# Optimization experiments

Measured on AMD Instinct MI355X. Metric: run time of the kernel, lower is better.

Reference implementation:

```python
import jax, jax.numpy as jnp
import numpy as np

NUM_NEGATIVES = 5  # global in original script
# TUPLE_OPTION == 'average', DATATYPE != 'clique' (tuplewise branch active)


def setup_inputs() -> dict:
    key = jax.random.key(0)
    k1, k2, k3 = jax.random.split(key, 3)
    N, D, P = 50000, 128, 8
    Q = NUM_NEGATIVES * P  # assert pos*NUM_NEGATIVES == neg in original
    return {
        "node_features": jax.random.normal(k1, (N, D), dtype=jnp.float32),
        "pos_idx": jax.random.randint(k2, (N, P), 0, N),
        "neg_idx": jax.random.randint(k3, (N, Q), 0, N),
        "hyperedge_node_idx": 10000,
    }


def reference(node_features, pos_idx, neg_idx, hyperedge_node_idx):
    x = node_features                      # [N, D]
    N = x.shape[0]
    P = pos_idx.shape[1]
    Q = neg_idx.shape[1]
    # per-node dot products with gathered neighbors, then sigmoid
    pos_s = jax.nn.sigmoid(jnp.einsum('nd,npd->np', x, x[pos_idx]))  # [N, P]
    neg_s = jax.nn.sigmoid(jnp.einsum('nd,nqd->nq', x, x[neg_idx]))  # [N, Q]
    # NOTE: original applies BCE-with-logits ON TOP of sigmoid scores (double
    # sigmoid) -- kept faithful. bce_logits(s, y) = softplus(s) - s*y
    per_node_pair = (
        (jax.nn.softplus(pos_s) - pos_s).sum(axis=1)  # labels = 1
        + jax.nn.softplus(neg_s).sum(axis=1)          # labels = 0
    ) / (P + Q)
    pairwise_loss = per_node_pair.mean()

    # tuplewise: reshape negs to (NUM_NEGATIVES, P) per node, average (TUPLE_OPTION='average')
    pos_t = pos_s.mean(axis=1)                                   # [N]
    neg_t = neg_s.reshape(N, NUM_NEGATIVES, P).mean(axis=2)      # [N, NUM_NEGATIVES]
    per_node_tuple = (
        jax.nn.softplus(pos_t) - pos_t
        + jax.nn.softplus(neg_t).sum(axis=1)
    ) / (1 + NUM_NEGATIVES)
    tuplewise_loss = per_node_tuple.sum() / (N - hyperedge_node_idx)

    return pairwise_loss + tuplewise_loss
```

## Files before the change

### kernel.cpp

```cpp
#include <hip/hip_runtime.h>

#define DIMS   128
#define PNUM   8
#define QNUM   40
#define NBR    48
#define WAVES_PER_BLOCK 4

typedef float f2 __attribute__((ext_vector_type(2)));

__global__ __launch_bounds__(256) void convert_f32_to_f8(
    const float* __restrict__ x, unsigned int* __restrict__ x8, int n8)
{
    const int stride = gridDim.x * blockDim.x;
    for (int i = blockIdx.x * blockDim.x + threadIdx.x; i < n8; i += stride) {
        const float4 v0 = reinterpret_cast<const float4*>(x)[2 * i];
        const float4 v1 = reinterpret_cast<const float4*>(x)[2 * i + 1];
        unsigned int a = __builtin_amdgcn_cvt_pk_fp8_f32(v0.x, v0.y, 0u, false);
        a = __builtin_amdgcn_cvt_pk_fp8_f32(v0.z, v0.w, a, true);
        unsigned int b = __builtin_amdgcn_cvt_pk_fp8_f32(v1.x, v1.y, 0u, false);
        b = __builtin_amdgcn_cvt_pk_fp8_f32(v1.z, v1.w, b, true);
        uint2 o; o.x = a; o.y = b;
        reinterpret_cast<uint2*>(x8)[i] = o;
    }
}

__device__ __forceinline__ float node_epilogue(float s, int lane, int N, int h)
{
    float pair_part = 0.0f;
    if (lane < NBR) {
        const float sp = __logf(1.0f + __expf(s));
        pair_part = (lane < PNUM) ? (sp - s) : sp;
    }
    float gs = s;
    gs += __shfl_xor(gs, 1);
    gs += __shfl_xor(gs, 2);
    gs += __shfl_xor(gs, 4);

    float tuple_part = 0.0f;
    if ((lane & 7) == 0 && lane < NBR) {
        const float t  = gs * 0.125f;
        const float sp = __logf(1.0f + __expf(t));
        tuple_part = (lane == 0) ? (sp - t) : sp;
    }
    const float pair_scale  = 1.0f / (48.0f * (float)N);
    const float tuple_scale = 1.0f / (6.0f  * (float)(N - h));
    return pair_part * pair_scale + tuple_part * tuple_scale;
}

__global__ __launch_bounds__(256) void node_loss_partial_f8v3(
    const float*        __restrict__ x,
    const unsigned int* __restrict__ x8,
    const int*          __restrict__ pos_idx,
    const int*          __restrict__ neg_idx,
    const int*          __restrict__ h_ptr,
    float*              __restrict__ ws,
    int N)
{
    __shared__ float scores_sh[WAVES_PER_BLOCK][NBR];
    __shared__ float wsum[WAVES_PER_BLOCK];

    const int wave = threadIdx.x >> 6;
    const int lane = threadIdx.x & 63;
    const int sub  = lane & 7;
    const int grp  = lane >> 3;
    const int node = blockIdx.x * WAVES_PER_BLOCK + wave;

    const int h = *h_ptr;

    float v = 0.0f;
    if (node < N) {
        int nb[6];
        nb[0] = pos_idx[node * PNUM + grp];
#pragma unroll
        for (int p = 1; p < 6; ++p)
            nb[p] = neg_idx[node * QNUM + (p - 1) * 8 + grp];

        const float4* own =
            reinterpret_cast<const float4*>(x + (size_t)node * DIMS) + sub * 4;
        const float4 f0 = own[0], f1 = own[1], f2v = own[2], f3 = own[3];

        uint4 q[6];
#pragma unroll
        for (int p = 0; p < 6; ++p)
            q[p] = *reinterpret_cast<const uint4*>(x8 + (size_t)nb[p] * 32 + sub * 4);

        f2 A2[8];
        A2[0] = f2{f0.x, f0.y};   A2[1] = f2{f0.z, f0.w};
        A2[2] = f2{f1.x, f1.y};   A2[3] = f2{f1.z, f1.w};
        A2[4] = f2{f2v.x, f2v.y}; A2[5] = f2{f2v.z, f2v.w};
        A2[6] = f2{f3.x, f3.y};   A2[7] = f2{f3.z, f3.w};

#pragma unroll
        for (int p = 0; p < 6; ++p) {
            f2 acc2 = {0.0f, 0.0f};
            acc2 += __builtin_amdgcn_cvt_pk_f32_fp8(q[p].x, false) * A2[0];
            acc2 += __builtin_amdgcn_cvt_pk_f32_fp8(q[p].x, true)  * A2[1];
            acc2 += __builtin_amdgcn_cvt_pk_f32_fp8(q[p].y, false) * A2[2];
            acc2 += __builtin_amdgcn_cvt_pk_f32_fp8(q[p].y, true)  * A2[3];
            acc2 += __builtin_amdgcn_cvt_pk_f32_fp8(q[p].z, false) * A2[4];
            acc2 += __builtin_amdgcn_cvt_pk_f32_fp8(q[p].z, true)  * A2[5];
            acc2 += __builtin_amdgcn_cvt_pk_f32_fp8(q[p].w, false) * A2[6];
            acc2 += __builtin_amdgcn_cvt_pk_f32_fp8(q[p].w, true)  * A2[7];
            float acc = acc2[0] + acc2[1];
            acc += __shfl_xor(acc, 1);
            acc += __shfl_xor(acc, 2);
            acc += __shfl_xor(acc, 4);
            if (sub == 0) scores_sh[wave][p * 8 + grp] = acc;
        }

        float s = 0.0f;
        if (lane < NBR) {
            const float sc = scores_sh[wave][lane];
            s = __builtin_amdgcn_rcpf(1.0f + __expf(-sc));
        }
        v = node_epilogue(s, lane, N, h);
    }

    v += __shfl_xor(v, 1);
    v += __shfl_xor(v, 2);
    v += __shfl_xor(v, 4);
    v += __shfl_xor(v, 8);
    v += __shfl_xor(v, 16);
    v += __shfl_xor(v, 32);

    if (lane == 0) wsum[wave] = v;
    __syncthreads();
    if (threadIdx.x == 0)
        ws[blockIdx.x] = wsum[0] + wsum[1] + wsum[2] + wsum[3];
}

__global__ __launch_bounds__(256) void node_loss_partial_f32(
    const float* __restrict__ x,
    const int*   __restrict__ pos_idx,
    const int*   __restrict__ neg_idx,
    const int*   __restrict__ h_ptr,
    float*       __restrict__ ws,
    int N)
{
    __shared__ float xn_sh[WAVES_PER_BLOCK][DIMS];
    __shared__ float wsum[WAVES_PER_BLOCK];

    const int wave = threadIdx.x >> 6;
    const int lane = threadIdx.x & 63;
    const int node = blockIdx.x * WAVES_PER_BLOCK + wave;

    if (node < N && lane < 32) {
        const float4* row = reinterpret_cast<const float4*>(x + (size_t)node * DIMS);
        reinterpret_cast<float4*>(xn_sh[wave])[lane] = row[lane];
    }
    __syncthreads();

    float v = 0.0f;
    if (node < N) {
        float s = 0.0f;
        if (lane < NBR) {
            const int nb = (lane < PNUM)
                ? pos_idx[node * PNUM + lane]
                : neg_idx[node * QNUM + (lane - PNUM)];
            const float4* nrow = reinterpret_cast<const float4*>(x + (size_t)nb * DIMS);
            const float4* xn4  = reinterpret_cast<const float4*>(xn_sh[wave]);
            float acc = 0.0f;
#pragma unroll
            for (int t = 0; t < DIMS / 4; ++t) {
                const float4 a = xn4[t];
                const float4 b = nrow[t];
                acc += a.x * b.x + a.y * b.y + a.z * b.z + a.w * b.w;
            }
            s = 1.0f / (1.0f + expf(-acc));
        }
        v = node_epilogue(s, lane, N, *h_ptr);
    }

    v += __shfl_xor(v, 1);
    v += __shfl_xor(v, 2);
    v += __shfl_xor(v, 4);
    v += __shfl_xor(v, 8);
    v += __shfl_xor(v, 16);
    v += __shfl_xor(v, 32);

    if (lane == 0) wsum[wave] = v;
    __syncthreads();
    if (threadIdx.x == 0)
        ws[blockIdx.x] = wsum[0] + wsum[1] + wsum[2] + wsum[3];
}

__global__ __launch_bounds__(256) void reduce_final(
    const float* __restrict__ ws, float* __restrict__ out, int nparts)
{
    __shared__ float sm[WAVES_PER_BLOCK];
    float acc = 0.0f;
    for (int i = threadIdx.x; i < nparts; i += 256) acc += ws[i];

    acc += __shfl_xor(acc, 1);
    acc += __shfl_xor(acc, 2);
    acc += __shfl_xor(acc, 4);
    acc += __shfl_xor(acc, 8);
    acc += __shfl_xor(acc, 16);
    acc += __shfl_xor(acc, 32);

    const int wave = threadIdx.x >> 6;
    const int lane = threadIdx.x & 63;
    if (lane == 0) sm[wave] = acc;
    __syncthreads();
    if (threadIdx.x == 0)
        out[0] = sm[0] + sm[1] + sm[2] + sm[3];
}

extern "C" void kernel_launch(void* const* d_in, const int* in_sizes, int n_in,
                              void* d_out, int out_size, void* d_ws, size_t ws_size,
                              hipStream_t stream) {
    const float* x   = (const float*)d_in[0];
    const int*   pos = (const int*)d_in[1];
    const int*   neg = (const int*)d_in[2];
    const int*   h   = (const int*)d_in[3];

    const int N = in_sizes[0] / DIMS;
    const int nblocks = (N + WAVES_PER_BLOCK - 1) / WAVES_PER_BLOCK;

    const size_t x8_bytes = (size_t)N * DIMS;
    const size_t need     = x8_bytes + (size_t)nblocks * sizeof(float);

    if (ws_size >= need) {
        unsigned int* x8 = (unsigned int*)d_ws;
        float* partials  = (float*)((char*)d_ws + x8_bytes);
        const int n8 = N * DIMS / 8;
        convert_f32_to_f8<<<2048, 256, 0, stream>>>(x, x8, n8);
        node_loss_partial_f8v3<<<nblocks, 256, 0, stream>>>(x, x8, pos, neg, h, partials, N);
        reduce_final<<<1, 256, 0, stream>>>(partials, (float*)d_out, nblocks);
    } else {
        float* partials = (float*)d_ws;
        node_loss_partial_f32<<<nblocks, 256, 0, stream>>>(x, pos, neg, h, partials, N);
        reduce_final<<<1, 256, 0, stream>>>(partials, (float*)d_out, nblocks);
    }
}
```

Baseline: 54.42 us.

## Compute per-node neighbor dot products with FP8 MFMA instead of VALU unpacking

Replaces the per-lane FP8 unpack-and-FMA dot products with 16x16x32 FP8 MFMA instructions. Each wave computes 48 neighbor scores as three 16-column tiles, reading the diagonal accumulator element, so the shared-memory score staging and shuffle reductions go away. The node's own row is now read from the FP8 copy rather than FP32, which cuts gather traffic but adds quantization error on both operands. The MFMA tiles compute a 16x16 product where only one row is needed, so most of the matrix work is discarded.

```diff
diff --git a/kernel.cpp b/kernel.cpp
--- a/kernel.cpp
+++ b/kernel.cpp
@@ -6,7 +6,7 @@
 #define NBR    48
 #define WAVES_PER_BLOCK 4
 
-typedef float f2 __attribute__((ext_vector_type(2)));
+typedef float f32x4 __attribute__((ext_vector_type(4)));
 
 __global__ __launch_bounds__(256) void convert_f32_to_f8(
     const float* __restrict__ x, unsigned int* __restrict__ x8, int n8)
@@ -47,70 +47,76 @@
     return pair_part * pair_scale + tuple_part * tuple_scale;
 }
 
-__global__ __launch_bounds__(256) void node_loss_partial_f8v3(
-    const float*        __restrict__ x,
-    const unsigned int* __restrict__ x8,
-    const int*          __restrict__ pos_idx,
-    const int*          __restrict__ neg_idx,
-    const int*          __restrict__ h_ptr,
-    float*              __restrict__ ws,
+__global__ __launch_bounds__(256) void node_loss_mfma_wave(
+    const unsigned char* __restrict__ x8,
+    const int*           __restrict__ pos_idx,
+    const int*           __restrict__ neg_idx,
+    const int*           __restrict__ h_ptr,
+    float*               __restrict__ ws,
     int N)
 {
-    __shared__ float scores_sh[WAVES_PER_BLOCK][NBR];
     __shared__ float wsum[WAVES_PER_BLOCK];
 
     const int wave = threadIdx.x >> 6;
     const int lane = threadIdx.x & 63;
-    const int sub  = lane & 7;
-    const int grp  = lane >> 3;
+    const int col  = lane & 15;
+    const int q    = lane >> 4;
     const int node = blockIdx.x * WAVES_PER_BLOCK + wave;
 
     const int h = *h_ptr;
 
     float v = 0.0f;
     if (node < N) {
-        int nb[6];
-        nb[0] = pos_idx[node * PNUM + grp];
-#pragma unroll
-        for (int p = 1; p < 6; ++p)
-            nb[p] = neg_idx[node * QNUM + (p - 1) * 8 + grp];
-
-        const float4* own =
-            reinterpret_cast<const float4*>(x + (size_t)node * DIMS) + sub * 4;
-        const float4 f0 = own[0], f1 = own[1], f2v = own[2], f3 = own[3];
-
-        uint4 q[6];
-#pragma unroll
-        for (int p = 0; p < 6; ++p)
-            q[p] = *reinterpret_cast<const uint4*>(x8 + (size_t)nb[p] * 32 + sub * 4);
-
-        f2 A2[8];
-        A2[0] = f2{f0.x, f0.y};   A2[1] = f2{f0.z, f0.w};
-        A2[2] = f2{f1.x, f1.y};   A2[3] = f2{f1.z, f1.w};
-        A2[4] = f2{f2v.x, f2v.y}; A2[5] = f2{f2v.z, f2v.w};
-        A2[6] = f2{f3.x, f3.y};   A2[7] = f2{f3.z, f3.w};
-
-#pragma unroll
-        for (int p = 0; p < 6; ++p) {
-            f2 acc2 = {0.0f, 0.0f};
-            acc2 += __builtin_amdgcn_cvt_pk_f32_fp8(q[p].x, false) * A2[0];
-            acc2 += __builtin_amdgcn_cvt_pk_f32_fp8(q[p].x, true)  * A2[1];
-            acc2 += __builtin_amdgcn_cvt_pk_f32_fp8(q[p].y, false) * A2[2];
-            acc2 += __builtin_amdgcn_cvt_pk_f32_fp8(q[p].y, true)  * A2[3];
-            acc2 += __builtin_amdgcn_cvt_pk_f32_fp8(q[p].z, false) * A2[4];
-            acc2 += __builtin_amdgcn_cvt_pk_f32_fp8(q[p].z, true)  * A2[5];
-            acc2 += __builtin_amdgcn_cvt_pk_f32_fp8(q[p].w, false) * A2[6];
-            acc2 += __builtin_amdgcn_cvt_pk_f32_fp8(q[p].w, true)  * A2[7];
-            float acc = acc2[0] + acc2[1];
-            acc += __shfl_xor(acc, 1);
-            acc += __shfl_xor(acc, 2);
-            acc += __shfl_xor(acc, 4);
-            if (sub == 0) scores_sh[wave][p * 8 + grp] = acc;
-        }
+        const int nb0 = (col < PNUM) ? pos_idx[node * PNUM + col]
+                                     : neg_idx[node * QNUM + (col - PNUM)];
+        const int nb1 = neg_idx[node * QNUM + 8 + col];
+        const int nb2 = neg_idx[node * QNUM + 24 + col];
+
+        const unsigned char* ap = x8 + (size_t)node * DIMS + q * 32;
+        const ulonglong2 a01 = *reinterpret_cast<const ulonglong2*>(ap);
+        const ulonglong2 a23 = *reinterpret_cast<const ulonglong2*>(ap + 16);
+
+        const unsigned char* b0p = x8 + (size_t)nb0 * DIMS + q * 32;
+        const unsigned char* b1p = x8 + (size_t)nb1 * DIMS + q * 32;
+        const unsigned char* b2p = x8 + (size_t)nb2 * DIMS + q * 32;
+        const ulonglong2 b0a = *reinterpret_cast<const ulonglong2*>(b0p);
+        const ulonglong2 b0b = *reinterpret_cast<const ulonglong2*>(b0p + 16);
+        const ulonglong2 b1a = *reinterpret_cast<const ulonglong2*>(b1p);
+        const ulonglong2 b1b = *reinterpret_cast<const ulonglong2*>(b1p + 16);
+        const ulonglong2 b2a = *reinterpret_cast<const ulonglong2*>(b2p);
+        const ulonglong2 b2b = *reinterpret_cast<const ulonglong2*>(b2p + 16);
+
+        f32x4 acc0 = {0.f, 0.f, 0.f, 0.f};
+        f32x4 acc1 = {0.f, 0.f, 0.f, 0.f};
+        f32x4 acc2 = {0.f, 0.f, 0.f, 0.f};
+        acc0 = __builtin_amdgcn_mfma_f32_16x16x32_fp8_fp8(
+            (long long)a01.x, (long long)b0a.x, acc0, 0, 0, 0);
+        acc1 = __builtin_amdgcn_mfma_f32_16x16x32_fp8_fp8(
+            (long long)a01.x, (long long)b1a.x, acc1, 0, 0, 0);
+        acc2 = __builtin_amdgcn_mfma_f32_16x16x32_fp8_fp8(
+            (long long)a01.x, (long long)b2a.x, acc2, 0, 0, 0);
+        acc0 = __builtin_amdgcn_mfma_f32_16x16x32_fp8_fp8(
+            (long long)a01.y, (long long)b0a.y, acc0, 0, 0, 0);
+        acc1 = __builtin_amdgcn_mfma_f32_16x16x32_fp8_fp8(
+            (long long)a01.y, (long long)b1a.y, acc1, 0, 0, 0);
+        acc2 = __builtin_amdgcn_mfma_f32_16x16x32_fp8_fp8(
+            (long long)a01.y, (long long)b2a.y, acc2, 0, 0, 0);
+        acc0 = __builtin_amdgcn_mfma_f32_16x16x32_fp8_fp8(
+            (long long)a23.x, (long long)b0b.x, acc0, 0, 0, 0);
+        acc1 = __builtin_amdgcn_mfma_f32_16x16x32_fp8_fp8(
+            (long long)a23.x, (long long)b1b.x, acc1, 0, 0, 0);
+        acc2 = __builtin_amdgcn_mfma_f32_16x16x32_fp8_fp8(
+            (long long)a23.x, (long long)b2b.x, acc2, 0, 0, 0);
+        acc0 = __builtin_amdgcn_mfma_f32_16x16x32_fp8_fp8(
+            (long long)a23.y, (long long)b0b.y, acc0, 0, 0, 0);
+        acc1 = __builtin_amdgcn_mfma_f32_16x16x32_fp8_fp8(
+            (long long)a23.y, (long long)b1b.y, acc1, 0, 0, 0);
+        acc2 = __builtin_amdgcn_mfma_f32_16x16x32_fp8_fp8(
+            (long long)a23.y, (long long)b2b.y, acc2, 0, 0, 0);
 
         float s = 0.0f;
         if (lane < NBR) {
-            const float sc = scores_sh[wave][lane];
+            const float sc = (q == 0) ? acc0[0] : (q == 1) ? acc1[0] : acc2[0];
             s = __builtin_amdgcn_rcpf(1.0f + __expf(-sc));
         }
         v = node_epilogue(s, lane, N, h);
@@ -221,11 +227,11 @@
     const size_t need     = x8_bytes + (size_t)nblocks * sizeof(float);
 
     if (ws_size >= need) {
-        unsigned int* x8 = (unsigned int*)d_ws;
-        float* partials  = (float*)((char*)d_ws + x8_bytes);
+        unsigned char* x8 = (unsigned char*)d_ws;
+        float* partials   = (float*)((char*)d_ws + x8_bytes);
         const int n8 = N * DIMS / 8;
-        convert_f32_to_f8<<<2048, 256, 0, stream>>>(x, x8, n8);
-        node_loss_partial_f8v3<<<nblocks, 256, 0, stream>>>(x, x8, pos, neg, h, partials, N);
+        convert_f32_to_f8<<<2048, 256, 0, stream>>>(x, (unsigned int*)x8, n8);
+        node_loss_mfma_wave<<<nblocks, 256, 0, stream>>>(x8, pos, neg, h, partials, N);
         reduce_final<<<1, 256, 0, stream>>>(partials, (float*)d_out, nblocks);
     } else {
         float* partials = (float*)d_ws;
```

New measurement: 65.30 us. 1.2x slower.

## Make fp8 loss kernel persistent with double-buffered gather prefetch

Applied to the files above, without the earlier changes.

The per-node fp8 loss kernel becomes a persistent grid of 1024 blocks. Each wave walks nodes with a grid stride and double-buffers the index, own-row and fp8 neighbour loads, so the next node's gathers are in flight while the current node is computed. This is meant to hide gather latency and cut block launch and partial-reduction overhead. The cost is higher register pressure from two buffer sets, which could lower occupancy.

```diff
diff --git a/kernel.cpp b/kernel.cpp
--- a/kernel.cpp
+++ b/kernel.cpp
@@ -4,7 +4,7 @@
 #define PNUM   8
 #define QNUM   40
 #define NBR    48
-#define WAVES_PER_BLOCK 4
+#define WPB    4
 
 typedef float f2 __attribute__((ext_vector_type(2)));
 
@@ -47,7 +47,62 @@
     return pair_part * pair_scale + tuple_part * tuple_scale;
 }
 
-__global__ __launch_bounds__(256) void node_loss_partial_f8v3(
+#define IDXLOAD(NB, ND)                                                       \
+    do {                                                                      \
+        NB[0] = pos_idx[(ND) * PNUM + grp];                                   \
+        _Pragma("unroll")                                                     \
+        for (int p_ = 1; p_ < 6; ++p_)                                        \
+            NB[p_] = neg_idx[(ND) * QNUM + (p_ - 1) * 8 + grp];               \
+    } while (0)
+
+#define OWNLOAD(OWN, ND)                                                      \
+    do {                                                                      \
+        const float4* o_ =                                                    \
+            reinterpret_cast<const float4*>(x + (size_t)(ND) * DIMS) + sub * 4;\
+        OWN[0] = o_[0]; OWN[1] = o_[1]; OWN[2] = o_[2]; OWN[3] = o_[3];       \
+    } while (0)
+
+#define GATHER(Q, NB)                                                         \
+    do {                                                                      \
+        _Pragma("unroll")                                                     \
+        for (int p_ = 0; p_ < 6; ++p_)                                        \
+            Q[p_] = *reinterpret_cast<const uint4*>(                          \
+                x8 + (size_t)NB[p_] * 32 + sub * 4);                          \
+    } while (0)
+
+#define COMPUTE(Q, OWN)                                                       \
+    do {                                                                      \
+        f2 A2[8];                                                             \
+        A2[0] = f2{OWN[0].x, OWN[0].y}; A2[1] = f2{OWN[0].z, OWN[0].w};       \
+        A2[2] = f2{OWN[1].x, OWN[1].y}; A2[3] = f2{OWN[1].z, OWN[1].w};       \
+        A2[4] = f2{OWN[2].x, OWN[2].y}; A2[5] = f2{OWN[2].z, OWN[2].w};       \
+        A2[6] = f2{OWN[3].x, OWN[3].y}; A2[7] = f2{OWN[3].z, OWN[3].w};       \
+        _Pragma("unroll")                                                     \
+        for (int p_ = 0; p_ < 6; ++p_) {                                      \
+            f2 acc2 = {0.0f, 0.0f};                                           \
+            acc2 += __builtin_amdgcn_cvt_pk_f32_fp8(Q[p_].x, false) * A2[0];  \
+            acc2 += __builtin_amdgcn_cvt_pk_f32_fp8(Q[p_].x, true)  * A2[1];  \
+            acc2 += __builtin_amdgcn_cvt_pk_f32_fp8(Q[p_].y, false) * A2[2];  \
+            acc2 += __builtin_amdgcn_cvt_pk_f32_fp8(Q[p_].y, true)  * A2[3];  \
+            acc2 += __builtin_amdgcn_cvt_pk_f32_fp8(Q[p_].z, false) * A2[4];  \
+            acc2 += __builtin_amdgcn_cvt_pk_f32_fp8(Q[p_].z, true)  * A2[5];  \
+            acc2 += __builtin_amdgcn_cvt_pk_f32_fp8(Q[p_].w, false) * A2[6];  \
+            acc2 += __builtin_amdgcn_cvt_pk_f32_fp8(Q[p_].w, true)  * A2[7];  \
+            float acc_ = acc2[0] + acc2[1];                                   \
+            acc_ += __shfl_xor(acc_, 1);                                      \
+            acc_ += __shfl_xor(acc_, 2);                                      \
+            acc_ += __shfl_xor(acc_, 4);                                      \
+            if (sub == 0) scores_sh[wave][p_ * 8 + grp] = acc_;               \
+        }                                                                     \
+        float s_ = 0.0f;                                                      \
+        if (lane < NBR) {                                                     \
+            const float sc_ = scores_sh[wave][lane];                          \
+            s_ = __builtin_amdgcn_rcpf(1.0f + __expf(-sc_));                  \
+        }                                                                     \
+        vacc += node_epilogue(s_, lane, N, h);                                \
+    } while (0)
+
+__global__ __launch_bounds__(256) void node_loss_persist(
     const float*        __restrict__ x,
     const unsigned int* __restrict__ x8,
     const int*          __restrict__ pos_idx,
@@ -56,74 +111,57 @@
     float*              __restrict__ ws,
     int N)
 {
-    __shared__ float scores_sh[WAVES_PER_BLOCK][NBR];
-    __shared__ float wsum[WAVES_PER_BLOCK];
+    __shared__ float scores_sh[WPB][NBR];
+    __shared__ float wsum[WPB];
 
     const int wave = threadIdx.x >> 6;
     const int lane = threadIdx.x & 63;
     const int sub  = lane & 7;
     const int grp  = lane >> 3;
-    const int node = blockIdx.x * WAVES_PER_BLOCK + wave;
-
-    const int h = *h_ptr;
-
-    float v = 0.0f;
-    if (node < N) {
-        int nb[6];
-        nb[0] = pos_idx[node * PNUM + grp];
-#pragma unroll
-        for (int p = 1; p < 6; ++p)
-            nb[p] = neg_idx[node * QNUM + (p - 1) * 8 + grp];
-
-        const float4* own =
-            reinterpret_cast<const float4*>(x + (size_t)node * DIMS) + sub * 4;
-        const float4 f0 = own[0], f1 = own[1], f2v = own[2], f3 = own[3];
-
-        uint4 q[6];
-#pragma unroll
-        for (int p = 0; p < 6; ++p)
-            q[p] = *reinterpret_cast<const uint4*>(x8 + (size_t)nb[p] * 32 + sub * 4);
-
-        f2 A2[8];
-        A2[0] = f2{f0.x, f0.y};   A2[1] = f2{f0.z, f0.w};
-        A2[2] = f2{f1.x, f1.y};   A2[3] = f2{f1.z, f1.w};
-        A2[4] = f2{f2v.x, f2v.y}; A2[5] = f2{f2v.z, f2v.w};
-        A2[6] = f2{f3.x, f3.y};   A2[7] = f2{f3.z, f3.w};
-
-#pragma unroll
-        for (int p = 0; p < 6; ++p) {
-            f2 acc2 = {0.0f, 0.0f};
-            acc2 += __builtin_amdgcn_cvt_pk_f32_fp8(q[p].x, false) * A2[0];
-            acc2 += __builtin_amdgcn_cvt_pk_f32_fp8(q[p].x, true)  * A2[1];
-            acc2 += __builtin_amdgcn_cvt_pk_f32_fp8(q[p].y, false) * A2[2];
-            acc2 += __builtin_amdgcn_cvt_pk_f32_fp8(q[p].y, true)  * A2[3];
-            acc2 += __builtin_amdgcn_cvt_pk_f32_fp8(q[p].z, false) * A2[4];
-            acc2 += __builtin_amdgcn_cvt_pk_f32_fp8(q[p].z, true)  * A2[5];
-            acc2 += __builtin_amdgcn_cvt_pk_f32_fp8(q[p].w, false) * A2[6];
-            acc2 += __builtin_amdgcn_cvt_pk_f32_fp8(q[p].w, true)  * A2[7];
-            float acc = acc2[0] + acc2[1];
-            acc += __shfl_xor(acc, 1);
-            acc += __shfl_xor(acc, 2);
-            acc += __shfl_xor(acc, 4);
-            if (sub == 0) scores_sh[wave][p * 8 + grp] = acc;
+    const int gs_  = gridDim.x * WPB;
+    const int h    = *h_ptr;
+
+    float vacc = 0.0f;
+
+    int C = blockIdx.x * WPB + wave;
+
+    int    nbA[6], nbB[6];
+    float4 ownA[4], ownB[4];
+    uint4  qA[6], qB[6];
+
+    if (C < N) {
+        IDXLOAD(nbA, C);
+        OWNLOAD(ownA, C);
+        if (C + gs_ < N) { IDXLOAD(nbB, C + gs_); OWNLOAD(ownB, C + gs_); }
+        GATHER(qA, nbA);
+    }
+
+    while (C < N) {
+        {
+            const int n1 = C + gs_, n2 = C + 2 * gs_;
+            if (n1 < N) GATHER(qB, nbB);
+            COMPUTE(qA, ownA);
+            if (n2 < N) { IDXLOAD(nbA, n2); OWNLOAD(ownA, n2); }
+            C = n1;
         }
-
-        float s = 0.0f;
-        if (lane < NBR) {
-            const float sc = scores_sh[wave][lane];
-            s = __builtin_amdgcn_rcpf(1.0f + __expf(-sc));
+        if (C >= N) break;
+        {
+            const int n1 = C + gs_, n2 = C + 2 * gs_;
+            if (n1 < N) GATHER(qA, nbA);
+            COMPUTE(qB, ownB);
+            if (n2 < N) { IDXLOAD(nbB, n2); OWNLOAD(ownB, n2); }
+            C = n1;
         }
-        v = node_epilogue(s, lane, N, h);
-    }
-
-    v += __shfl_xor(v, 1);
-    v += __shfl_xor(v, 2);
-    v += __shfl_xor(v, 4);
-    v += __shfl_xor(v, 8);
-    v += __shfl_xor(v, 16);
-    v += __shfl_xor(v, 32);
-
-    if (lane == 0) wsum[wave] = v;
+    }
+
+    vacc += __shfl_xor(vacc, 1);
+    vacc += __shfl_xor(vacc, 2);
+    vacc += __shfl_xor(vacc, 4);
+    vacc += __shfl_xor(vacc, 8);
+    vacc += __shfl_xor(vacc, 16);
+    vacc += __shfl_xor(vacc, 32);
+
+    if (lane == 0) wsum[wave] = vacc;
     __syncthreads();
     if (threadIdx.x == 0)
         ws[blockIdx.x] = wsum[0] + wsum[1] + wsum[2] + wsum[3];
@@ -137,12 +175,12 @@
     float*       __restrict__ ws,
     int N)
 {
-    __shared__ float xn_sh[WAVES_PER_BLOCK][DIMS];
-    __shared__ float wsum[WAVES_PER_BLOCK];
+    __shared__ float xn_sh[WPB][DIMS];
+    __shared__ float wsum[WPB];
 
     const int wave = threadIdx.x >> 6;
     const int lane = threadIdx.x & 63;
-    const int node = blockIdx.x * WAVES_PER_BLOCK + wave;
+    const int node = blockIdx.x * WPB + wave;
 
     if (node < N && lane < 32) {
         const float4* row = reinterpret_cast<const float4*>(x + (size_t)node * DIMS);
@@ -187,7 +225,7 @@
 __global__ __launch_bounds__(256) void reduce_final(
     const float* __restrict__ ws, float* __restrict__ out, int nparts)
 {
-    __shared__ float sm[WAVES_PER_BLOCK];
+    __shared__ float sm[WPB];
     float acc = 0.0f;
     for (int i = threadIdx.x; i < nparts; i += 256) acc += ws[i];
 
@@ -215,20 +253,21 @@
     const int*   h   = (const int*)d_in[3];
 
     const int N = in_sizes[0] / DIMS;
-    const int nblocks = (N + WAVES_PER_BLOCK - 1) / WAVES_PER_BLOCK;
 
     const size_t x8_bytes = (size_t)N * DIMS;
-    const size_t need     = x8_bytes + (size_t)nblocks * sizeof(float);
+    const int    PBLOCKS  = 1024;
+    const size_t need     = x8_bytes + (size_t)PBLOCKS * sizeof(float);
 
     if (ws_size >= need) {
         unsigned int* x8 = (unsigned int*)d_ws;
         float* partials  = (float*)((char*)d_ws + x8_bytes);
         const int n8 = N * DIMS / 8;
         convert_f32_to_f8<<<2048, 256, 0, stream>>>(x, x8, n8);
-        node_loss_partial_f8v3<<<nblocks, 256, 0, stream>>>(x, x8, pos, neg, h, partials, N);
-        reduce_final<<<1, 256, 0, stream>>>(partials, (float*)d_out, nblocks);
+        node_loss_persist<<<PBLOCKS, 256, 0, stream>>>(x, x8, pos, neg, h, partials, N);
+        reduce_final<<<1, 256, 0, stream>>>(partials, (float*)d_out, PBLOCKS);
     } else {
         float* partials = (float*)d_ws;
+        const int nblocks = (N + WPB - 1) / WPB;
         node_loss_partial_f32<<<nblocks, 256, 0, stream>>>(x, pos, neg, h, partials, N);
         reduce_final<<<1, 256, 0, stream>>>(partials, (float*)d_out, nblocks);
     }
```

After: 62.71 us. 15.2% more time.
